# Kernel tuning notes

Measured on AMD Instinct MI355X. Metric: run time of the kernel, lower is better.

The kernel has to match this reference:

```python
import jax, jax.numpy as jnp
import numpy as np

D = 2048; H = 16; KV = 4; HD = D // H  # head_dim=128
EPS = 1e-6; THETA = 10000.0


def _rmsnorm(x, w):
    # x: [..., HD]
    var = jnp.mean(x * x, axis=-1, keepdims=True)
    return x * jax.lax.rsqrt(var + EPS) * w


def _rope(x, cos, sin):
    # x: [B, L, nH, HD]; cos/sin: [L, HD//2]; interleaved-pair rotation
    xe = x[..., 0::2]
    xo = x[..., 1::2]
    c = cos[None, :, None, :]
    s = sin[None, :, None, :]
    re = xe * c - xo * s
    ro = xe * s + xo * c
    return jnp.stack([re, ro], axis=-1).reshape(x.shape)


def setup_inputs() -> dict:
    key = jax.random.key(0)
    ks = jax.random.split(key, 8)
    B, L = 2, 2048
    x = jax.random.normal(ks[0], (B, L, D), dtype=jnp.float32)
    wq = jax.random.normal(ks[1], (D, D), dtype=jnp.float32) * 0.02
    wk = jax.random.normal(ks[2], (KV * HD, D), dtype=jnp.float32) * 0.02
    wv = jax.random.normal(ks[3], (KV * HD, D), dtype=jnp.float32) * 0.02
    wo = jax.random.normal(ks[4], (D, D), dtype=jnp.float32) * 0.02
    q_norm_w = jnp.ones((HD,), dtype=jnp.float32)
    k_norm_w = jnp.ones((HD,), dtype=jnp.float32)
    return {"x": x, "wq": wq, "wk": wk, "wv": wv, "wo": wo,
            "q_norm_w": q_norm_w, "k_norm_w": k_norm_w}


def reference(x, wq, wk, wv, wo, q_norm_w, k_norm_w):
    B, L, _ = x.shape
    G = H // KV  # GQA group size (repeat factor)

    q = (x @ wq.T).reshape(B, L, H, HD)
    k = (x @ wk.T).reshape(B, L, KV, HD)
    v = (x @ wv.T).reshape(B, L, KV, HD)

    q = _rmsnorm(q, q_norm_w)
    k = _rmsnorm(k, k_norm_w)

    # RoPE (positions 0..L-1, prompt path)
    inv_freq = 1.0 / (THETA ** (jnp.arange(0, HD, 2, dtype=jnp.float32) / HD))
    ang = jnp.arange(L, dtype=jnp.float32)[:, None] * inv_freq[None, :]  # [L, HD/2]
    cos, sin = jnp.cos(ang), jnp.sin(ang)
    q = _rope(q, cos, sin)
    k = _rope(k, cos, sin)

    # GQA: q head h attends kv head h // G (== repeat_interleave of k,v)
    qg = q.reshape(B, L, KV, G, HD)
    scale = 1.0 / jnp.sqrt(jnp.float32(HD))
    scores = jnp.einsum('bqkgd,bskd->bkgqs', qg, k) * scale  # [B,KV,G,L,L]

    causal = jnp.tril(jnp.ones((L, L), dtype=bool))
    scores = jnp.where(causal, scores, jnp.finfo(scores.dtype).min)
    p = jax.nn.softmax(scores, axis=-1)

    o = jnp.einsum('bkgqs,bskd->bqkgd', p, v).reshape(B, L, D)
    return o @ wo.T
```

## Files before the change

kernel.cpp:

```cpp
#include <hip/hip_runtime.h>
#include <hip/hip_bf16.h>
#include <stdint.h>
#include <stddef.h>

#define D_DIM 2048
#define H_HEADS 16
#define KV_HEADS 4
#define HEAD_DIM 128
#define SEQ_L 2048
#define BATCH 2
#define NTOK 4096
#define NQK 2560
#define NQKV 3072

typedef __attribute__((ext_vector_type(4))) float f32x4;
typedef __attribute__((ext_vector_type(16))) float f32x16;
typedef __attribute__((ext_vector_type(8))) short bf16x8;

__device__ __forceinline__ unsigned short f2bf(float f) {
  __hip_bfloat16 h = __float2bfloat16(f);
  return *reinterpret_cast<unsigned short*>(&h);
}
__device__ __forceinline__ unsigned pack2(float lo, float hi) {
  return (unsigned)f2bf(lo) | ((unsigned)f2bf(hi) << 16);
}
__device__ __forceinline__ float bf2f(unsigned short s) {
  return __uint_as_float(((unsigned int)s) << 16);
}

__device__ __forceinline__ void async_copy16(const void* g, void* l) {
  __builtin_amdgcn_global_load_lds(
      (__attribute__((address_space(1))) void*)(g),
      (__attribute__((address_space(3))) void*)(l),
      16, 0, 0);
}

__device__ __forceinline__ void cast_seg(const float* __restrict__ src,
                                         unsigned short* __restrict__ dst,
                                         int n4, int gid, int stride) {
  for (int i = gid; i < n4; i += stride) {
    float4 v = *reinterpret_cast<const float4*>(src + i * 4);
    uint2 o;
    o.x = pack2(v.x, v.y);
    o.y = pack2(v.z, v.w);
    *reinterpret_cast<uint2*>(dst + i * 4) = o;
  }
}

__global__ __launch_bounds__(256) void fused_cast_kernel(
    const float* __restrict__ s0, const float* __restrict__ s1,
    const float* __restrict__ s2, const float* __restrict__ s3,
    const float* __restrict__ s4,
    unsigned short* __restrict__ d0, unsigned short* __restrict__ d1,
    unsigned short* __restrict__ d2, unsigned short* __restrict__ d3,
    unsigned short* __restrict__ d4) {
  int gid = blockIdx.x * blockDim.x + threadIdx.x;
  int stride = gridDim.x * blockDim.x;
  cast_seg(s0, d0, (NTOK * D_DIM) / 4, gid, stride);
  cast_seg(s1, d1, (D_DIM * D_DIM) / 4, gid, stride);
  cast_seg(s2, d2, (512 * D_DIM) / 4, gid, stride);
  cast_seg(s3, d3, (512 * D_DIM) / 4, gid, stride);
  cast_seg(s4, d4, (D_DIM * D_DIM) / 4, gid, stride);
}

__global__ __launch_bounds__(256) void rope_table_kernel(float* __restrict__ cosT,
                                                         float* __restrict__ sinT) {
  int i = blockIdx.x * blockDim.x + threadIdx.x;
  if (i >= SEQ_L * 64) return;
  int p = i & 63;
  float l = (float)(i >> 6);
  float inv = powf(10000.0f, -(float)p / 64.0f);
  float ang = l * inv;
  cosT[i] = cosf(ang);
  sinT[i] = sinf(ang);
}

__device__ __forceinline__ void store_out(unsigned short* p, float v) { *p = f2bf(v); }
__device__ __forceinline__ void store_out(float* p, float v) { *p = v; }

template <typename OutT, bool VSPLIT>
__global__ __launch_bounds__(256) void gemm_bt_kernel(const unsigned short* __restrict__ A,
                                                      const unsigned short* __restrict__ B,
                                                      OutT* __restrict__ C,
                                                      unsigned short* __restrict__ vt,
                                                      int M, int N, int K) {
  __shared__ unsigned short Alds[128 * 32];
  __shared__ unsigned short Blds[128 * 32];
  const int tid = threadIdx.x;
  const int wave = tid >> 6;
  const int lane = tid & 63;
  const int l15 = lane & 15;
  const int l4 = lane >> 4;

  const int nwg = gridDim.x * gridDim.y;
  const int orig = blockIdx.y * gridDim.x + blockIdx.x;
  const int cpx = nwg >> 3;
  const int swz = (orig & 7) * cpx + (orig >> 3);
  const int m0 = (swz % gridDim.x) * 128;
  const int n0 = (swz / gridDim.x) * 128;

  const int wm = (wave >> 1) * 64;
  const int wn = (wave & 1) * 64;

  f32x4 acc[4][4] = {};

  const int soff0 = wave * 1024 + lane * 16;

  for (int kt = 0; kt < K; kt += 32) {
#pragma unroll
    for (int inst = 0; inst < 2; ++inst) {
      int off = soff0 + inst * 4096;
      int row = off >> 6;
      int colb = off & 63;
      const char* ga = (const char*)(A + (size_t)(m0 + row) * K + kt) + colb;
      async_copy16(ga, (char*)Alds + off);
      const char* gb = (const char*)(B + (size_t)(n0 + row) * K + kt) + colb;
      async_copy16(gb, (char*)Blds + off);
    }
    __syncthreads();
    bf16x8 af[4], bfr[4];
#pragma unroll
    for (int i = 0; i < 4; ++i)
      af[i] = *reinterpret_cast<const bf16x8*>(Alds + (wm + i * 16 + l15) * 32 + l4 * 8);
#pragma unroll
    for (int j = 0; j < 4; ++j)
      bfr[j] = *reinterpret_cast<const bf16x8*>(Blds + (wn + j * 16 + l15) * 32 + l4 * 8);
#pragma unroll
    for (int i = 0; i < 4; ++i)
#pragma unroll
      for (int j = 0; j < 4; ++j)
        acc[i][j] = __builtin_amdgcn_mfma_f32_16x16x32_bf16(af[i], bfr[j], acc[i][j], 0, 0, 0);
    __syncthreads();
  }

  if (VSPLIT && n0 >= NQK) {
#pragma unroll
    for (int i = 0; i < 4; ++i)
#pragma unroll
      for (int j = 0; j < 4; ++j) {
        int vrow = n0 + wn + j * 16 + l15 - NQK;
        int tok0 = m0 + wm + i * 16 + l4 * 4;
        ushort4 pk;
        pk.x = f2bf(acc[i][j][0]);
        pk.y = f2bf(acc[i][j][1]);
        pk.z = f2bf(acc[i][j][2]);
        pk.w = f2bf(acc[i][j][3]);
        *reinterpret_cast<ushort4*>(vt + (size_t)vrow * NTOK + tok0) = pk;
      }
    return;
  }

  const int cstride = VSPLIT ? NQK : N;
#pragma unroll
  for (int i = 0; i < 4; ++i)
#pragma unroll
    for (int j = 0; j < 4; ++j) {
      int col = n0 + wn + j * 16 + l15;
#pragma unroll
      for (int r = 0; r < 4; ++r) {
        int row = m0 + wm + i * 16 + l4 * 4 + r;
        store_out(C + (size_t)row * cstride + col, acc[i][j][r]);
      }
    }
}

__global__ __launch_bounds__(256) void norm_rope_kernel(unsigned short* __restrict__ qk,
                                                        const float* __restrict__ qw,
                                                        const float* __restrict__ kw,
                                                        const float* __restrict__ cosT,
                                                        const float* __restrict__ sinT) {
  int wid = (blockIdx.x * blockDim.x + threadIdx.x) >> 6;
  int lane = threadIdx.x & 63;
  unsigned short* rowp;
  const float* w;
  int m;
  float sc;
  if (wid < NTOK * H_HEADS) {
    m = wid >> 4;
    int hh = wid & 15;
    rowp = qk + (size_t)m * NQK + hh * HEAD_DIM;
    w = qw;
    sc = 0.08838834764831845f;
  } else {
    int r2 = wid - NTOK * H_HEADS;
    m = r2 >> 2;
    int kvh = r2 & 3;
    rowp = qk + (size_t)m * NQK + D_DIM + kvh * HEAD_DIM;
    w = kw;
    sc = 1.0f;
  }
  int l = m & (SEQ_L - 1);
  unsigned int pair = *reinterpret_cast<const unsigned int*>(rowp + lane * 2);
  float e = bf2f((unsigned short)(pair & 0xffffu));
  float o = bf2f((unsigned short)(pair >> 16));
  float ss = e * e + o * o;
#pragma unroll
  for (int off = 1; off < 64; off <<= 1) ss += __shfl_xor(ss, off);
  float rsn = rsqrtf(ss * (1.0f / 128.0f) + 1e-6f) * sc;
  float we = w[lane * 2], wo_ = w[lane * 2 + 1];
  float c = cosT[l * 64 + lane], s = sinT[l * 64 + lane];
  float xe = e * rsn * we, xo = o * rsn * wo_;
  float re = xe * c - xo * s;
  float ro = xe * s + xo * c;
  *reinterpret_cast<unsigned int*>(rowp + lane * 2) = pack2(re, ro);
}

__global__ __launch_bounds__(256, 2) void attn_kernel(const unsigned short* __restrict__ qk,
                                                      const unsigned short* __restrict__ vt,
                                                      unsigned short* __restrict__ obuf) {
  __shared__ unsigned short Kl[2][64 * 128];
  __shared__ unsigned short Vl[2][128 * 64];
  __shared__ float invl[128];

  const int tid = threadIdx.x;
  const int w = tid >> 6, lane = tid & 63;
  const int l31 = lane & 31, hi = lane >> 5;
  const int qt = gridDim.x - 1 - blockIdx.x;
  const int q0 = qt * 128;
  const int bh = blockIdx.y;
  const int b = bh >> 4, h = bh & 15, kvh = h >> 2;

  const unsigned short* Qg = qk + (size_t)(b * SEQ_L + q0 + w * 32 + l31) * NQK + h * HEAD_DIM;
  const unsigned short* Kg = qk + (size_t)(b * SEQ_L) * NQK + D_DIM + kvh * HEAD_DIM;
  const unsigned short* Vg = vt + (size_t)(kvh * HEAD_DIM) * NTOK + b * SEQ_L;

  bf16x8 qf[8];
#pragma unroll
  for (int kk = 0; kk < 8; ++kk)
    qf[kk] = *reinterpret_cast<const bf16x8*>(Qg + kk * 16 + hi * 8);

  f32x16 accO[4] = {};
  float m_run = -1e30f, l_run = 0.0f;

  const int qmin_w = q0 + w * 32;
  const int qmax_w = qmin_w + 31;
  const int qg = qmin_w + l31;
  const int ntiles = (q0 + 128) >> 6;

  auto stage = [&](int bb, int kt) {
#pragma unroll
    for (int i = 0; i < 4; ++i) {
      int o = (i * 256 + tid) * 16;
      {
        int row = o >> 8;
        int scb = (o & 255) ^ ((row & 7) << 4);
        const char* src = (const char*)(Kg + (size_t)(kt * 64 + row) * NQK) + scb;
        async_copy16(src, (char*)(&Kl[bb][0]) + o);
      }
      {
        int d = o >> 7;
        int skb = (o & 127) ^ ((d & 7) << 4);
        const char* src = (const char*)(Vg + (size_t)d * NTOK + kt * 64) + skb;
        async_copy16(src, (char*)(&Vl[bb][0]) + o);
      }
    }
  };

  stage(0, 0);
  asm volatile("s_waitcnt vmcnt(0)" ::: "memory");
  __syncthreads();

  int buf = 0;
  for (int kt = 0; kt < ntiles; ++kt) {
    if (kt + 1 < ntiles) stage(buf ^ 1, kt + 1);

    if (kt * 64 <= qmax_w) {
      f32x16 st[2] = {};
      __builtin_amdgcn_s_setprio(1);
#pragma unroll
      for (int stile = 0; stile < 2; ++stile) {
#pragma unroll
        for (int kk = 0; kk < 8; ++kk) {
          int row = stile * 32 + l31;
          int off = (row << 8) + (((kk << 5) + (hi << 4)) ^ ((l31 & 7) << 4));
          bf16x8 kf = *reinterpret_cast<const bf16x8*>((const char*)(&Kl[buf][0]) + off);
          st[stile] = __builtin_amdgcn_mfma_f32_32x32x16_bf16(kf, qf[kk], st[stile], 0, 0, 0);
        }
      }
      __builtin_amdgcn_s_setprio(0);

      const bool need_mask = (kt * 64 + 63 > qmin_w);
      float tmax = -1e30f;
#pragma unroll
      for (int stile = 0; stile < 2; ++stile)
#pragma unroll
        for (int r = 0; r < 16; ++r) {
          float s = st[stile][r];
          if (need_mask) {
            int key = kt * 64 + stile * 32 + (r & 3) + ((r >> 2) << 3) + (hi << 2);
            if (key > qg) s = -1e30f;
          }
          st[stile][r] = s;
          tmax = fmaxf(tmax, s);
        }
      tmax = fmaxf(tmax, __shfl_xor(tmax, 32));

      if (!__all(tmax - m_run <= 8.0f)) {
        float mnew = fmaxf(m_run, tmax);
        float corr = __expf(m_run - mnew);
        m_run = mnew;
        l_run *= corr;
        float corrq[16];
#pragma unroll
        for (int r = 0; r < 16; ++r) {
          int qi = (r & 3) + ((r >> 2) << 3) + (hi << 2);
          corrq[r] = __shfl(corr, qi);
        }
#pragma unroll
        for (int dt = 0; dt < 4; ++dt)
#pragma unroll
          for (int r = 0; r < 16; ++r) accO[dt][r] *= corrq[r];
      }

      float rsum = 0.0f;
#pragma unroll
      for (int stile = 0; stile < 2; ++stile)
#pragma unroll
        for (int r = 0; r < 16; ++r) {
          float pe = __expf(st[stile][r] - m_run);
          st[stile][r] = pe;
          rsum += pe;
        }
      rsum += __shfl_xor(rsum, 32);
      l_run += rsum;

      bf16x8 pa[2][2];
#pragma unroll
      for (int stile = 0; stile < 2; ++stile)
#pragma unroll
        for (int kc = 0; kc < 2; ++kc) {
          int rb = kc * 8;
          unsigned x0 = pack2(st[stile][rb + 0], st[stile][rb + 1]);
          unsigned y0 = pack2(st[stile][rb + 4], st[stile][rb + 5]);
          unsigned x1 = pack2(st[stile][rb + 2], st[stile][rb + 3]);
          unsigned y1 = pack2(st[stile][rb + 6], st[stile][rb + 7]);
          unsigned x0s = (unsigned)__shfl_xor((int)x0, 32);
          unsigned y0s = (unsigned)__shfl_xor((int)y0, 32);
          unsigned x1s = (unsigned)__shfl_xor((int)x1, 32);
          unsigned y1s = (unsigned)__shfl_xor((int)y1, 32);
          unsigned w0 = hi ? y0s : x0;
          unsigned w2 = hi ? y0 : x0s;
          unsigned w1 = hi ? y1s : x1;
          unsigned w3 = hi ? y1 : x1s;
          union { bf16x8 v; unsigned u[4]; } uu;
          uu.u[0] = w0; uu.u[1] = w1; uu.u[2] = w2; uu.u[3] = w3;
          pa[stile][kc] = uu.v;
        }

      __builtin_amdgcn_s_setprio(1);
#pragma unroll
      for (int dt = 0; dt < 4; ++dt) {
        int drow = dt * 32 + l31;
#pragma unroll
        for (int stile = 0; stile < 2; ++stile)
#pragma unroll
          for (int kc = 0; kc < 2; ++kc) {
            int off = (drow << 7) + (((stile << 6) + (kc << 5) + (hi << 4)) ^ ((l31 & 7) << 4));
            bf16x8 vf = *reinterpret_cast<const bf16x8*>((const char*)(&Vl[buf][0]) + off);
            accO[dt] = __builtin_amdgcn_mfma_f32_32x32x16_bf16(pa[stile][kc], vf, accO[dt], 0, 0, 0);
          }
      }
      __builtin_amdgcn_s_setprio(0);
    }

    asm volatile("s_waitcnt vmcnt(0)" ::: "memory");
    __syncthreads();
    buf ^= 1;
  }

  if (hi == 0) invl[w * 32 + l31] = 1.0f / l_run;
  __syncthreads();
#pragma unroll
  for (int dt = 0; dt < 4; ++dt)
#pragma unroll
    for (int r = 0; r < 16; ++r) {
      int qrow = (r & 3) + ((r >> 2) << 3) + (hi << 2);
      float val = accO[dt][r] * invl[w * 32 + qrow];
      int tok = b * SEQ_L + q0 + w * 32 + qrow;
      obuf[(size_t)tok * D_DIM + h * HEAD_DIM + dt * 32 + l31] = f2bf(val);
    }
}

extern "C" void kernel_launch(void* const* d_in, const int* in_sizes, int n_in,
                              void* d_out, int out_size, void* d_ws, size_t ws_size,
                              hipStream_t stream) {
  const float* x   = (const float*)d_in[0];
  const float* wq  = (const float*)d_in[1];
  const float* wk  = (const float*)d_in[2];
  const float* wv  = (const float*)d_in[3];
  const float* wo  = (const float*)d_in[4];
  const float* qnw = (const float*)d_in[5];
  const float* knw = (const float*)d_in[6];
  float* out = (float*)d_out;

  char* ws = (char*)d_ws;
  unsigned short* Xb    = (unsigned short*)(ws);
  unsigned short* Wqkvb = (unsigned short*)(ws + 16777216);
  unsigned short* Wob   = (unsigned short*)(ws + 29360128);
  unsigned short* QKb   = (unsigned short*)(ws + 37748736);
  unsigned short* VTb   = (unsigned short*)(ws + 58720256);
  unsigned short* Obuf  = (unsigned short*)(ws + 62914560);
  float* cosT = (float*)(ws + 79691776);
  float* sinT = (float*)(ws + 80216064);

  fused_cast_kernel<<<1024, 256, 0, stream>>>(
      x, wq, wk, wv, wo,
      Xb, Wqkvb,
      Wqkvb + (size_t)D_DIM * D_DIM,
      Wqkvb + (size_t)NQK * D_DIM,
      Wob);
  rope_table_kernel<<<512, 256, 0, stream>>>(cosT, sinT);

  dim3 g1(NTOK / 128, NQKV / 128);
  gemm_bt_kernel<unsigned short, true><<<g1, 256, 0, stream>>>(
      Xb, Wqkvb, QKb, VTb, NTOK, NQKV, D_DIM);

  norm_rope_kernel<<<(NTOK * (H_HEADS + KV_HEADS)) / 4, 256, 0, stream>>>(QKb, qnw, knw, cosT, sinT);

  attn_kernel<<<dim3(SEQ_L / 128, BATCH * H_HEADS), 256, 0, stream>>>(QKb, VTb, Obuf);

  dim3 g2(NTOK / 128, D_DIM / 128);
  gemm_bt_kernel<float, false><<<g2, 256, 0, stream>>>(Obuf, Wob, out, nullptr, NTOK, D_DIM, D_DIM);
}
```

Measured before the change: 260.3 us.

## Split long causal query tiles across two KV segments with a combine pass

Query tiles 8-15 now have their KV range split into two halves, each processed by a separate block, so the grid grows from 16 to 24 blocks per head and the work per block is more even under the causal mask. The first segment writes its unnormalized output to Obuf and the second to a scratch buffer, each along with per-row max and sum. A new combine kernel merges the two halves with log-sum-exp weights. This adds a kernel launch and extra global traffic, rounds the partials to bf16, and reuses the workspace region that held the X cast, which is assumed dead by this point.

```diff
diff --git a/kernel.cpp b/kernel.cpp
--- a/kernel.cpp
+++ b/kernel.cpp
@@ -207,7 +207,10 @@
 
 __global__ __launch_bounds__(256, 2) void attn_kernel(const unsigned short* __restrict__ qk,
                                                       const unsigned short* __restrict__ vt,
-                                                      unsigned short* __restrict__ obuf) {
+                                                      unsigned short* __restrict__ obuf,
+                                                      unsigned short* __restrict__ p2,
+                                                      float* __restrict__ m1G, float* __restrict__ l1G,
+                                                      float* __restrict__ m2G, float* __restrict__ l2G) {
   __shared__ unsigned short Kl[2][64 * 128];
   __shared__ unsigned short Vl[2][128 * 64];
   __shared__ float invl[128];
@@ -215,8 +218,26 @@
   const int tid = threadIdx.x;
   const int w = tid >> 6, lane = tid & 63;
   const int l31 = lane & 31, hi = lane >> 5;
-  const int qt = gridDim.x - 1 - blockIdx.x;
+
+  const int jx = blockIdx.x;
+  int qt, seg, kv_begin, kv_end;
+  bool split;
+  if (jx < 16) {
+    split = true;
+    qt = 15 - (jx >> 1);
+    seg = jx & 1;
+    int nt = qt + 1;
+    kv_begin = seg * nt;
+    kv_end = kv_begin + nt;
+  } else {
+    split = false;
+    seg = 0;
+    qt = 23 - jx;
+    kv_begin = 0;
+    kv_end = 2 * qt + 2;
+  }
   const int q0 = qt * 128;
+
   const int bh = blockIdx.y;
   const int b = bh >> 4, h = bh & 15, kvh = h >> 2;
 
@@ -235,7 +256,6 @@
   const int qmin_w = q0 + w * 32;
   const int qmax_w = qmin_w + 31;
   const int qg = qmin_w + l31;
-  const int ntiles = (q0 + 128) >> 6;
 
   auto stage = [&](int bb, int kt) {
 #pragma unroll
@@ -256,13 +276,13 @@
     }
   };
 
-  stage(0, 0);
+  stage(0, kv_begin);
   asm volatile("s_waitcnt vmcnt(0)" ::: "memory");
   __syncthreads();
 
   int buf = 0;
-  for (int kt = 0; kt < ntiles; ++kt) {
-    if (kt + 1 < ntiles) stage(buf ^ 1, kt + 1);
+  for (int kt = kv_begin; kt < kv_end; ++kt) {
+    if (kt + 1 < kv_end) stage(buf ^ 1, kt + 1);
 
     if (kt * 64 <= qmax_w) {
       f32x16 st[2] = {};
@@ -368,17 +388,78 @@
     buf ^= 1;
   }
 
-  if (hi == 0) invl[w * 32 + l31] = 1.0f / l_run;
-  __syncthreads();
-#pragma unroll
-  for (int dt = 0; dt < 4; ++dt)
-#pragma unroll
-    for (int r = 0; r < 16; ++r) {
-      int qrow = (r & 3) + ((r >> 2) << 3) + (hi << 2);
-      float val = accO[dt][r] * invl[w * 32 + qrow];
-      int tok = b * SEQ_L + q0 + w * 32 + qrow;
-      obuf[(size_t)tok * D_DIM + h * HEAD_DIM + dt * 32 + l31] = f2bf(val);
+  if (!split) {
+    if (hi == 0) invl[w * 32 + l31] = 1.0f / l_run;
+    __syncthreads();
+#pragma unroll
+    for (int dt = 0; dt < 4; ++dt)
+#pragma unroll
+      for (int r = 0; r < 16; ++r) {
+        int qrow = (r & 3) + ((r >> 2) << 3) + (hi << 2);
+        float val = accO[dt][r] * invl[w * 32 + qrow];
+        int tok = b * SEQ_L + q0 + w * 32 + qrow;
+        obuf[(size_t)tok * D_DIM + h * HEAD_DIM + dt * 32 + l31] = f2bf(val);
+      }
+  } else {
+    const int rowbase = bh * 1024 + (qt - 8) * 128;
+    if (hi == 0) {
+      int rr = rowbase + w * 32 + l31;
+      if (seg == 0) { m1G[rr] = m_run; l1G[rr] = l_run; }
+      else          { m2G[rr] = m_run; l2G[rr] = l_run; }
     }
+#pragma unroll
+    for (int dt = 0; dt < 4; ++dt)
+#pragma unroll
+      for (int r = 0; r < 16; ++r) {
+        int qrow = (r & 3) + ((r >> 2) << 3) + (hi << 2);
+        float val = accO[dt][r];
+        if (seg == 0) {
+          int tok = b * SEQ_L + q0 + w * 32 + qrow;
+          obuf[(size_t)tok * D_DIM + h * HEAD_DIM + dt * 32 + l31] = f2bf(val);
+        } else {
+          size_t prow = (size_t)(rowbase + w * 32 + qrow);
+          p2[prow * HEAD_DIM + dt * 32 + l31] = f2bf(val);
+        }
+      }
+  }
+}
+
+__global__ __launch_bounds__(256) void combine_kernel(unsigned short* __restrict__ obuf,
+                                                      const unsigned short* __restrict__ p2,
+                                                      const float* __restrict__ m1G, const float* __restrict__ l1G,
+                                                      const float* __restrict__ m2G, const float* __restrict__ l2G) {
+  int gid = blockIdx.x * blockDim.x + threadIdx.x;
+  int row = gid >> 4;
+  int dc = (gid & 15) * 8;
+  int bh = row >> 10;
+  int rem = row & 1023;
+  int qt = 8 + (rem >> 7);
+  int rr = rem & 127;
+  int b = bh >> 4, h = bh & 15;
+  size_t tok = (size_t)(b * SEQ_L + qt * 128 + rr);
+
+  float m1 = m1G[row], l1 = l1G[row], m2 = m2G[row], l2 = l2G[row];
+  float mm = fmaxf(m1, m2);
+  float w1 = __expf(m1 - mm), w2 = __expf(m2 - mm);
+  float inv = 1.0f / (w1 * l1 + w2 * l2);
+
+  unsigned short* op = obuf + tok * D_DIM + h * HEAD_DIM + dc;
+  const unsigned short* pp = p2 + (size_t)row * HEAD_DIM + dc;
+  ushort4 a0 = *reinterpret_cast<const ushort4*>(op);
+  ushort4 a1 = *reinterpret_cast<const ushort4*>(op + 4);
+  ushort4 b0 = *reinterpret_cast<const ushort4*>(pp);
+  ushort4 b1 = *reinterpret_cast<const ushort4*>(pp + 4);
+  ushort4 o0, o1;
+  o0.x = f2bf((w1 * bf2f(a0.x) + w2 * bf2f(b0.x)) * inv);
+  o0.y = f2bf((w1 * bf2f(a0.y) + w2 * bf2f(b0.y)) * inv);
+  o0.z = f2bf((w1 * bf2f(a0.z) + w2 * bf2f(b0.z)) * inv);
+  o0.w = f2bf((w1 * bf2f(a0.w) + w2 * bf2f(b0.w)) * inv);
+  o1.x = f2bf((w1 * bf2f(a1.x) + w2 * bf2f(b1.x)) * inv);
+  o1.y = f2bf((w1 * bf2f(a1.y) + w2 * bf2f(b1.y)) * inv);
+  o1.z = f2bf((w1 * bf2f(a1.z) + w2 * bf2f(b1.z)) * inv);
+  o1.w = f2bf((w1 * bf2f(a1.w) + w2 * bf2f(b1.w)) * inv);
+  *reinterpret_cast<ushort4*>(op) = o0;
+  *reinterpret_cast<ushort4*>(op + 4) = o1;
 }
 
 extern "C" void kernel_launch(void* const* d_in, const int* in_sizes, int n_in,
@@ -403,6 +484,12 @@
   float* cosT = (float*)(ws + 79691776);
   float* sinT = (float*)(ws + 80216064);
 
+  unsigned short* P2 = (unsigned short*)(ws);
+  float* m1G = (float*)(ws + 8388608);
+  float* l1G = (float*)(ws + 8519680);
+  float* m2G = (float*)(ws + 8650752);
+  float* l2G = (float*)(ws + 8781824);
+
   fused_cast_kernel<<<1024, 256, 0, stream>>>(
       x, wq, wk, wv, wo,
       Xb, Wqkvb,
@@ -417,7 +504,9 @@
 
   norm_rope_kernel<<<(NTOK * (H_HEADS + KV_HEADS)) / 4, 256, 0, stream>>>(QKb, qnw, knw, cosT, sinT);
 
-  attn_kernel<<<dim3(SEQ_L / 128, BATCH * H_HEADS), 256, 0, stream>>>(QKb, VTb, Obuf);
+  attn_kernel<<<dim3(24, BATCH * H_HEADS), 256, 0, stream>>>(
+      QKb, VTb, Obuf, P2, m1G, l1G, m2G, l2G);
+  combine_kernel<<<2048, 256, 0, stream>>>(Obuf, P2, m1G, l1G, m2G, l2G);
 
   dim3 g2(NTOK / 128, D_DIM / 128);
   gemm_bt_kernel<float, false><<<g2, 256, 0, stream>>>(Obuf, Wob, out, nullptr, NTOK, D_DIM, D_DIM);
```

Result: no change. 261.6 us (+0.5%).
